# Kernel optimization log

Measured on AMD Instinct MI355X. Metric: run time of the kernel, lower is better.

The kernel has to match this reference:

```python
import jax, jax.numpy as jnp
import numpy as np

B, H_WIN, W_WIN = 2048, 8, 8
N = H_WIN * W_WIN            # tokens per window = 64
C = 384                      # channels
HEADS, HEAD_DIM = 12, 32
E = HEADS * HEAD_DIM         # embedding channels = 384
EPS = 1e-5


def _relative_position_indices(h, w):
    coords = np.stack(np.meshgrid(np.arange(h), np.arange(w), indexing='ij')).reshape(2, -1)  # [2, N]
    rel = coords[:, :, None] - coords[:, None, :]      # [2, N, N]
    rel = rel.transpose(1, 2, 0).astype(np.int64)      # [N, N, 2]
    rel[..., 0] = (rel[..., 0] + h - 1) * (2 * w - 1)
    rel[..., 1] += w - 1
    return rel.sum(-1)                                 # [N, N] in [0, (2h-1)(2w-1))


def setup_inputs() -> dict:
    key = jax.random.key(0)
    ks = jax.random.split(key, 6)
    x = jax.random.normal(ks[0], (B, N, C), dtype=jnp.float32)
    ln_g = jnp.ones((C,), jnp.float32)
    ln_b = jnp.zeros((C,), jnp.float32)
    w_qkv = jax.random.normal(ks[1], (3 * E, C), jnp.float32) * (1.0 / np.sqrt(C))
    w_out = jax.random.normal(ks[2], (C, E), jnp.float32) * (1.0 / np.sqrt(E))
    b_out = jnp.zeros((C,), jnp.float32)
    n_bias = (2 * H_WIN - 1) * (2 * W_WIN - 1)
    bias_table = jax.random.truncated_normal(ks[3], -2.0, 2.0, (n_bias, HEADS), jnp.float32) * 0.02
    rel_idx = jnp.asarray(_relative_position_indices(H_WIN, W_WIN))  # [N, N] int64
    return {"x": x, "ln_g": ln_g, "ln_b": ln_b, "w_qkv": w_qkv,
            "w_out": w_out, "b_out": b_out, "bias_table": bias_table, "rel_idx": rel_idx}


def reference(x, ln_g, ln_b, w_qkv, w_out, b_out, bias_table, rel_idx):
    # pre-norm
    mu = jnp.mean(x, axis=-1, keepdims=True)
    var = jnp.var(x, axis=-1, keepdims=True)
    xn = (x - mu) * jax.lax.rsqrt(var + EPS) * ln_g + ln_b
    # qkv projection (no bias)
    qkv = jnp.einsum('bnc,ec->bne', xn, w_qkv)                     # [B, N, 3E]
    qkv = qkv.reshape(x.shape[0], N, 3, HEADS, HEAD_DIM)
    q, k, v = (qkv[:, :, i].transpose(0, 2, 1, 3) for i in range(3))  # each [B, h, N, d]
    scale = 1.0 / np.sqrt(HEAD_DIM)
    scores = jnp.einsum('bhnd,bhmd->bhnm', q * scale, k)           # [B, h, N, N]
    # gather learned relative-position bias per (n, m) pair
    bias = bias_table[rel_idx]                                     # [N, N, h]
    scores = scores + bias.transpose(2, 0, 1)[None]                # broadcast over B
    p = jax.nn.softmax(scores, axis=-1)
    out = jnp.einsum('bhnm,bhmd->bhnd', p, v)                      # [B, h, N, d]
    out = out.transpose(0, 2, 1, 3).reshape(x.shape[0], N, E)
    return jnp.einsum('bne,ce->bnc', out, w_out) + b_out
```

## Files before the change

kernel.cpp:

```cpp
#include <hip/hip_runtime.h>
#include <hip/hip_bf16.h>


#define NTOK  64
#define CCH   384
#define NH    12
#define HD    32
#define EPSV  1e-5f
#define SCALEQ 0.17677669529663687f

#define WQP_ELEMS (72 * 12 * 64 * 8)
#define WOP_ELEMS (24 * 12 * 64 * 8)
#define BLUTP_ELEMS (12 * 4 * 4 * 64 * 4)

typedef __attribute__((ext_vector_type(8))) short  short8;
typedef __attribute__((ext_vector_type(4))) short  short4v;
typedef __attribute__((ext_vector_type(4))) float  float4v;
typedef __attribute__((ext_vector_type(4))) int    int4v;

__device__ __forceinline__ unsigned short f2bf(float f) {
    union { float f; unsigned int i; } v; v.f = f;
    unsigned int r = v.i + 0x7fffu + ((v.i >> 16) & 1u);
    return (unsigned short)(r >> 16);
}
__device__ __forceinline__ unsigned int pack2bf(float lo, float hi) {
    return (unsigned int)f2bf(lo) | ((unsigned int)f2bf(hi) << 16);
}

__global__ void prep_kernel(const float* __restrict__ w_qkv_f,
                            const float* __restrict__ w_out_f,
                            const float* __restrict__ bias_tab,
                            const int*   __restrict__ rel_idx,
                            unsigned short* __restrict__ wqp,
                            unsigned short* __restrict__ wop,
                            float* __restrict__ blutp) {
    const int stride = gridDim.x * blockDim.x;
    const int tid = blockIdx.x * blockDim.x + threadIdx.x;
    for (int i = tid; i < WQP_ELEMS; i += stride) {
        const int t = i / 6144, rem = i % 6144;
        const int kk = rem >> 9, rem2 = rem & 511;
        const int lane = rem2 >> 3, e = rem2 & 7;
        wqp[i] = f2bf(w_qkv_f[(16 * t + (lane & 15)) * CCH + 32 * kk + 8 * (lane >> 4) + e]);
    }
    for (int i = tid; i < WOP_ELEMS; i += stride) {
        const int t = i / 6144, rem = i % 6144;
        const int kk = rem >> 9, rem2 = rem & 511;
        const int lane = rem2 >> 3, e = rem2 & 7;
        wop[i] = f2bf(w_out_f[(16 * t + (lane & 15)) * CCH + 32 * kk + 8 * (lane >> 4) + e]);
    }
    for (int i = tid; i < BLUTP_ELEMS; i += stride) {
        const int r = i & 3, lane = (i >> 2) & 63;
        const int kt = (i >> 8) & 3, tt = (i >> 10) & 3, h = i >> 12;
        const int token = 16 * tt + (lane & 15);
        const int key   = 16 * kt + 4 * (lane >> 4) + r;
        blutp[i] = bias_tab[rel_idx[token * 64 + key] * NH + h];
    }
}

__global__ __launch_bounds__(512, 2)
void fused_win_mha(const float* __restrict__ x,
                   const float* __restrict__ ln_g,
                   const float* __restrict__ ln_b,
                   const float* __restrict__ b_out,
                   const unsigned short* __restrict__ wqp,
                   const unsigned short* __restrict__ wop,
                   const float* __restrict__ blutp,
                   float* __restrict__ out)
{
    const int b    = blockIdx.x;
    const int t    = threadIdx.x;
    const int wav  = t >> 6;
    const int lane = t & 63;
    const int l4   = lane >> 4;
    const int lc   = lane & 15;
    const int lh   = wav >> 1;
    const int mh   = wav & 1;

    __shared__ unsigned short xnp[4 * 12 * 64 * 8];
    __shared__ unsigned short qp [4 * 4 * 64 * 8];
    __shared__ unsigned short kp [4 * 4 * 64 * 8];
    __shared__ unsigned short vp [4 * 2 * 2 * 64 * 8];
    __shared__ unsigned short attp[4 * 4 * 64 * 8];

    {
        const int row = t >> 3, seg = t & 7;
        const float* xr = x + (b * NTOK + row) * CCH + seg * 48;
        float vals[48];
        float s = 0.f, s2 = 0.f;
        #pragma unroll
        for (int i = 0; i < 12; ++i) {
            float4v v = *(const float4v*)(xr + i * 4);
            #pragma unroll
            for (int j = 0; j < 4; ++j) {
                float f = v[j];
                vals[i * 4 + j] = f; s += f; s2 += f * f;
            }
        }
        s += __shfl_xor(s, 1); s2 += __shfl_xor(s2, 1);
        s += __shfl_xor(s, 2); s2 += __shfl_xor(s2, 2);
        s += __shfl_xor(s, 4); s2 += __shfl_xor(s2, 4);
        const float mu   = s * (1.f / CCH);
        const float rstd = rsqrtf(s2 * (1.f / CCH) - mu * mu + EPSV);
        #pragma unroll
        for (int u = 0; u < 6; ++u) {
            const int col0 = seg * 48 + u * 8;
            short8 w;
            #pragma unroll
            for (int e2 = 0; e2 < 2; ++e2) {
                float4v gv = *(const float4v*)(ln_g + col0 + e2 * 4);
                float4v bv = *(const float4v*)(ln_b + col0 + e2 * 4);
                #pragma unroll
                for (int j = 0; j < 4; ++j)
                    w[e2 * 4 + j] = (short)f2bf((vals[u * 8 + e2 * 4 + j] - mu) * rstd * gv[j] + bv[j]);
            }
            const int idx = ((((row >> 4) * 12 + (col0 >> 5)) << 9)
                             + ((((col0 >> 3) & 3) * 16 + (row & 15)) << 3));
            *(short8*)&xnp[idx] = w;
        }
    }
    __syncthreads();

    float4v facc[4][3];
    #pragma unroll
    for (int mt = 0; mt < 4; ++mt)
        #pragma unroll
        for (int j = 0; j < 3; ++j)
            facc[mt][j] = (float4v){0.f, 0.f, 0.f, 0.f};

    auto do_gemm2 = [&](int g) {
        #pragma unroll
        for (int ks = 0; ks < 4; ++ks) {
            short8 aG[4];
            #pragma unroll
            for (int mt = 0; mt < 4; ++mt)
                aG[mt] = *(const short8*)&attp[((mt * 4 + ks) << 9) + (lane << 3)];
            #pragma unroll
            for (int j2 = 0; j2 < 3; ++j2) {
                const int tile = 3 * wav + j2;
                short8 bG = *(const short8*)&wop[((tile * 12 + 4 * g + ks) << 9) + (lane << 3)];
                #pragma unroll
                for (int mt = 0; mt < 4; ++mt)
                    facc[mt][j2] = __builtin_amdgcn_mfma_f32_16x16x32_bf16(aG[mt], bG, facc[mt][j2], 0, 0, 0);
            }
        }
    };

    for (int grp = 0; grp < 3; ++grp) {
        const int h = 4 * grp + lh;

        if (grp > 0) do_gemm2(grp - 1);

        float4v acc[3][4];
        #pragma unroll
        for (int n = 0; n < 3; ++n)
            #pragma unroll
            for (int m = 0; m < 4; ++m)
                acc[n][m] = (float4v){0.f, 0.f, 0.f, 0.f};

        int tile_[3], mat_[3], half_[3];
        #pragma unroll
        for (int ntl = 0; ntl < 3; ++ntl) {
            const int part = 3 * mh + ntl;
            mat_[ntl] = part >> 1; half_[ntl] = part & 1;
            tile_[ntl] = mat_[ntl] * 24 + h * 2 + half_[ntl];
        }
        for (int kk = 0; kk < 12; ++kk) {
            short8 aF[4];
            #pragma unroll
            for (int mt = 0; mt < 4; ++mt)
                aF[mt] = *(const short8*)&xnp[(((mt * 12 + kk) << 9)) + (lane << 3)];
            #pragma unroll
            for (int ntl = 0; ntl < 3; ++ntl) {
                short8 bF = *(const short8*)&wqp[((tile_[ntl] * 12 + kk) << 9) + (lane << 3)];
                #pragma unroll
                for (int mt = 0; mt < 4; ++mt)
                    acc[ntl][mt] = __builtin_amdgcn_mfma_f32_16x16x32_bf16(aF[mt], bF, acc[ntl][mt], 0, 0, 0);
            }
        }

        float4v bb[2][4];
        #pragma unroll
        for (int j = 0; j < 2; ++j)
            #pragma unroll
            for (int kt = 0; kt < 4; ++kt)
                bb[j][kt] = *(const float4v*)(blutp + ((((h * 4 + (2 * mh + j)) * 4 + kt) << 6) + lane) * 4);

        #pragma unroll
        for (int ntl = 0; ntl < 3; ++ntl) {
            const int mat = mat_[ntl], half = half_[ntl];
            #pragma unroll
            for (int mt = 0; mt < 4; ++mt) {
                if (mat == 0) {
                    const int base = ((lh * 4 + mt) << 9) + ((2 * half + (lc >> 3)) << 7) + (lc & 7);
                    #pragma unroll
                    for (int r = 0; r < 4; ++r)
                        qp[base + ((4 * l4 + r) << 3)] = f2bf(acc[ntl][mt][r] * SCALEQ);
                } else if (mat == 1) {
                    const int base = ((lh * 4 + mt) << 9) + ((2 * half + (lc >> 3)) << 7) + (lc & 7);
                    #pragma unroll
                    for (int r = 0; r < 4; ++r)
                        kp[base + ((4 * l4 + r) << 3)] = f2bf(acc[ntl][mt][r]);
                } else {
                    short4v pk4;
                    #pragma unroll
                    for (int r = 0; r < 4; ++r)
                        pk4[r] = (short)f2bf(acc[ntl][mt][r]);
                    const int addr = (((lh * 2 + half) * 2 + (mt >> 1)) << 9)
                                   + ((((mt & 1) * 2 + (l4 >> 1)) * 16 + lc) << 3)
                                   + ((l4 & 1) << 2);
                    *(short4v*)&vp[addr] = pk4;
                }
            }
        }
        __syncthreads();

        float sv[2][4][4];
        #pragma unroll
        for (int j = 0; j < 2; ++j) {
            short8 qf = *(const short8*)&qp[((lh * 4 + (2 * mh + j)) << 9) + (lane << 3)];
            #pragma unroll
            for (int kt = 0; kt < 4; ++kt) {
                short8 kf = *(const short8*)&kp[((lh * 4 + kt) << 9) + (lane << 3)];
                float4v sres = __builtin_amdgcn_mfma_f32_16x16x32_bf16(
                    kf, qf, (float4v){0.f, 0.f, 0.f, 0.f}, 0, 0, 0);
                #pragma unroll
                for (int r = 0; r < 4; ++r) sv[j][kt][r] = sres[r];
            }
        }
        unsigned int pk2[2][4][2];
        #pragma unroll
        for (int j = 0; j < 2; ++j) {
            float m = -1e30f;
            #pragma unroll
            for (int kt = 0; kt < 4; ++kt) {
                #pragma unroll
                for (int r = 0; r < 4; ++r) {
                    sv[j][kt][r] += bb[j][kt][r];
                    m = fmaxf(m, sv[j][kt][r]);
                }
            }
            m = fmaxf(m, __shfl_xor(m, 16));
            m = fmaxf(m, __shfl_xor(m, 32));
            float s = 0.f;
            #pragma unroll
            for (int kt = 0; kt < 4; ++kt)
                #pragma unroll
                for (int r = 0; r < 4; ++r) {
                    float pe = __expf(sv[j][kt][r] - m);
                    sv[j][kt][r] = pe; s += pe;
                }
            s += __shfl_xor(s, 16);
            s += __shfl_xor(s, 32);
            const float rinv = 1.f / s;
            #pragma unroll
            for (int kt = 0; kt < 4; ++kt) {
                pk2[j][kt][0] = pack2bf(sv[j][kt][0] * rinv, sv[j][kt][1] * rinv);
                pk2[j][kt][1] = pack2bf(sv[j][kt][2] * rinv, sv[j][kt][3] * rinv);
            }
        }
        short8 af[2][2];
        {
            const int src0 = lc + 16 * (2 * (l4 & 1));
            const int src1 = src0 + 16;
            const bool hi  = ((l4 >> 1) & 1) != 0;
            #pragma unroll
            for (int j = 0; j < 2; ++j) {
                #pragma unroll
                for (int kk2 = 0; kk2 < 2; ++kk2) {
                    const int ka = 2 * kk2, kb = 2 * kk2 + 1;
                    unsigned int a0a = (unsigned int)__shfl((int)pk2[j][ka][0], src0);
                    unsigned int a0b = (unsigned int)__shfl((int)pk2[j][kb][0], src0);
                    unsigned int a1a = (unsigned int)__shfl((int)pk2[j][ka][1], src0);
                    unsigned int a1b = (unsigned int)__shfl((int)pk2[j][kb][1], src0);
                    unsigned int a2a = (unsigned int)__shfl((int)pk2[j][ka][0], src1);
                    unsigned int a2b = (unsigned int)__shfl((int)pk2[j][kb][0], src1);
                    unsigned int a3a = (unsigned int)__shfl((int)pk2[j][ka][1], src1);
                    unsigned int a3b = (unsigned int)__shfl((int)pk2[j][kb][1], src1);
                    int4v iv;
                    iv[0] = (int)(hi ? a0b : a0a);
                    iv[1] = (int)(hi ? a1b : a1a);
                    iv[2] = (int)(hi ? a2b : a2a);
                    iv[3] = (int)(hi ? a3b : a3a);
                    af[j][kk2] = __builtin_bit_cast(short8, iv);
                }
            }
        }

        float4v o[2][2];
        #pragma unroll
        for (int j = 0; j < 2; ++j)
            #pragma unroll
            for (int nt = 0; nt < 2; ++nt)
                o[j][nt] = (float4v){0.f, 0.f, 0.f, 0.f};
        #pragma unroll
        for (int kk2 = 0; kk2 < 2; ++kk2) {
            #pragma unroll
            for (int nt = 0; nt < 2; ++nt) {
                short8 vf = *(const short8*)&vp[(((lh * 2 + nt) * 2 + kk2) << 9) + (lane << 3)];
                #pragma unroll
                for (int j = 0; j < 2; ++j)
                    o[j][nt] = __builtin_amdgcn_mfma_f32_16x16x32_bf16(af[j][kk2], vf, o[j][nt], 0, 0, 0);
            }
        }
        #pragma unroll
        for (int j = 0; j < 2; ++j) {
            #pragma unroll
            for (int nt = 0; nt < 2; ++nt) {
                const int base = (((2 * mh + j) * 4 + lh) << 9) + ((2 * nt + (lc >> 3)) << 7) + (lc & 7);
                #pragma unroll
                for (int r = 0; r < 4; ++r)
                    attp[base + ((4 * l4 + r) << 3)] = f2bf(o[j][nt][r]);
            }
        }
        __syncthreads();
    }
    do_gemm2(2);

    {
        float* ob = out + b * (NTOK * CCH);
        #pragma unroll
        for (int mt = 0; mt < 4; ++mt) {
            #pragma unroll
            for (int j2 = 0; j2 < 3; ++j2) {
                const int c = 16 * (3 * wav + j2) + lc;
                const float bo = b_out[c];
                #pragma unroll
                for (int r = 0; r < 4; ++r)
                    ob[(16 * mt + 4 * l4 + r) * CCH + c] = facc[mt][j2][r] + bo;
            }
        }
    }
}

extern "C" void kernel_launch(void* const* d_in, const int* in_sizes, int n_in,
                              void* d_out, int out_size, void* d_ws, size_t ws_size,
                              hipStream_t stream) {
    const float* x     = (const float*)d_in[0];
    const float* ln_g  = (const float*)d_in[1];
    const float* ln_b  = (const float*)d_in[2];
    const float* w_qkv = (const float*)d_in[3];
    const float* w_out = (const float*)d_in[4];
    const float* b_out = (const float*)d_in[5];
    const float* btab  = (const float*)d_in[6];
    const int*   ridx  = (const int*)d_in[7];
    float*       out   = (float*)d_out;

    unsigned short* wqp   = (unsigned short*)d_ws;
    unsigned short* wop   = wqp + WQP_ELEMS;
    float*          blutp = (float*)(wop + WOP_ELEMS);

    prep_kernel<<<512, 256, 0, stream>>>(w_qkv, w_out, btab, ridx, wqp, wop, blutp);
    fused_win_mha<<<2048, 512, 0, stream>>>(x, ln_g, ln_b, b_out, wqp, wop, blutp, out);
}
```

Measured before the change: 342.3 us.

## Software-pipeline QKV GEMM with previous group's softmax, PV and output GEMM

Result: faster. 315.2 us (-7.9%).

```diff
diff --git a/kernel.cpp b/kernel.cpp
--- a/kernel.cpp
+++ b/kernel.cpp
@@ -127,139 +127,37 @@
         for (int j = 0; j < 3; ++j)
             facc[mt][j] = (float4v){0.f, 0.f, 0.f, 0.f};
 
-    auto do_gemm2 = [&](int g) {
-        #pragma unroll
-        for (int ks = 0; ks < 4; ++ks) {
-            short8 aG[4];
-            #pragma unroll
-            for (int mt = 0; mt < 4; ++mt)
-                aG[mt] = *(const short8*)&attp[((mt * 4 + ks) << 9) + (lane << 3)];
-            #pragma unroll
-            for (int j2 = 0; j2 < 3; ++j2) {
-                const int tile = 3 * wav + j2;
-                short8 bG = *(const short8*)&wop[((tile * 12 + 4 * g + ks) << 9) + (lane << 3)];
-                #pragma unroll
-                for (int mt = 0; mt < 4; ++mt)
-                    facc[mt][j2] = __builtin_amdgcn_mfma_f32_16x16x32_bf16(aG[mt], bG, facc[mt][j2], 0, 0, 0);
-            }
-        }
-    };
-
-    for (int grp = 0; grp < 3; ++grp) {
-        const int h = 4 * grp + lh;
-
-        if (grp > 0) do_gemm2(grp - 1);
-
-        float4v acc[3][4];
-        #pragma unroll
-        for (int n = 0; n < 3; ++n)
-            #pragma unroll
-            for (int m = 0; m < 4; ++m)
-                acc[n][m] = (float4v){0.f, 0.f, 0.f, 0.f};
-
-        int tile_[3], mat_[3], half_[3];
-        #pragma unroll
-        for (int ntl = 0; ntl < 3; ++ntl) {
-            const int part = 3 * mh + ntl;
-            mat_[ntl] = part >> 1; half_[ntl] = part & 1;
-            tile_[ntl] = mat_[ntl] * 24 + h * 2 + half_[ntl];
-        }
-        for (int kk = 0; kk < 12; ++kk) {
-            short8 aF[4];
-            #pragma unroll
-            for (int mt = 0; mt < 4; ++mt)
-                aF[mt] = *(const short8*)&xnp[(((mt * 12 + kk) << 9)) + (lane << 3)];
-            #pragma unroll
-            for (int ntl = 0; ntl < 3; ++ntl) {
-                short8 bF = *(const short8*)&wqp[((tile_[ntl] * 12 + kk) << 9) + (lane << 3)];
-                #pragma unroll
-                for (int mt = 0; mt < 4; ++mt)
-                    acc[ntl][mt] = __builtin_amdgcn_mfma_f32_16x16x32_bf16(aF[mt], bF, acc[ntl][mt], 0, 0, 0);
-            }
-        }
-
-        float4v bb[2][4];
-        #pragma unroll
-        for (int j = 0; j < 2; ++j)
-            #pragma unroll
-            for (int kt = 0; kt < 4; ++kt)
-                bb[j][kt] = *(const float4v*)(blutp + ((((h * 4 + (2 * mh + j)) * 4 + kt) << 6) + lane) * 4);
-
-        #pragma unroll
-        for (int ntl = 0; ntl < 3; ++ntl) {
-            const int mat = mat_[ntl], half = half_[ntl];
-            #pragma unroll
-            for (int mt = 0; mt < 4; ++mt) {
-                if (mat == 0) {
-                    const int base = ((lh * 4 + mt) << 9) + ((2 * half + (lc >> 3)) << 7) + (lc & 7);
-                    #pragma unroll
-                    for (int r = 0; r < 4; ++r)
-                        qp[base + ((4 * l4 + r) << 3)] = f2bf(acc[ntl][mt][r] * SCALEQ);
-                } else if (mat == 1) {
-                    const int base = ((lh * 4 + mt) << 9) + ((2 * half + (lc >> 3)) << 7) + (lc & 7);
-                    #pragma unroll
-                    for (int r = 0; r < 4; ++r)
-                        kp[base + ((4 * l4 + r) << 3)] = f2bf(acc[ntl][mt][r]);
-                } else {
-                    short4v pk4;
-                    #pragma unroll
-                    for (int r = 0; r < 4; ++r)
-                        pk4[r] = (short)f2bf(acc[ntl][mt][r]);
-                    const int addr = (((lh * 2 + half) * 2 + (mt >> 1)) << 9)
-                                   + ((((mt & 1) * 2 + (l4 >> 1)) * 16 + lc) << 3)
-                                   + ((l4 & 1) << 2);
-                    *(short4v*)&vp[addr] = pk4;
-                }
-            }
-        }
-        __syncthreads();
-
-        float sv[2][4][4];
-        #pragma unroll
-        for (int j = 0; j < 2; ++j) {
-            short8 qf = *(const short8*)&qp[((lh * 4 + (2 * mh + j)) << 9) + (lane << 3)];
-            #pragma unroll
-            for (int kt = 0; kt < 4; ++kt) {
-                short8 kf = *(const short8*)&kp[((lh * 4 + kt) << 9) + (lane << 3)];
-                float4v sres = __builtin_amdgcn_mfma_f32_16x16x32_bf16(
-                    kf, qf, (float4v){0.f, 0.f, 0.f, 0.f}, 0, 0, 0);
-                #pragma unroll
-                for (int r = 0; r < 4; ++r) sv[j][kt][r] = sres[r];
-            }
-        }
-        unsigned int pk2[2][4][2];
-        #pragma unroll
-        for (int j = 0; j < 2; ++j) {
-            float m = -1e30f;
-            #pragma unroll
-            for (int kt = 0; kt < 4; ++kt) {
-                #pragma unroll
-                for (int r = 0; r < 4; ++r) {
-                    sv[j][kt][r] += bb[j][kt][r];
-                    m = fmaxf(m, sv[j][kt][r]);
-                }
-            }
-            m = fmaxf(m, __shfl_xor(m, 16));
-            m = fmaxf(m, __shfl_xor(m, 32));
-            float s = 0.f;
-            #pragma unroll
-            for (int kt = 0; kt < 4; ++kt)
-                #pragma unroll
-                for (int r = 0; r < 4; ++r) {
-                    float pe = __expf(sv[j][kt][r] - m);
-                    sv[j][kt][r] = pe; s += pe;
-                }
-            s += __shfl_xor(s, 16);
-            s += __shfl_xor(s, 32);
-            const float rinv = 1.f / s;
-            #pragma unroll
-            for (int kt = 0; kt < 4; ++kt) {
-                pk2[j][kt][0] = pack2bf(sv[j][kt][0] * rinv, sv[j][kt][1] * rinv);
-                pk2[j][kt][1] = pack2bf(sv[j][kt][2] * rinv, sv[j][kt][3] * rinv);
-            }
-        }
+    float sv[2][4][4];
+    float mx[2];
+
+    #pragma unroll
+    for (int it = 0; it < 4; ++it) {
         short8 af[2][2];
-        {
+        if (it > 0) {
+            unsigned int pk2[2][4][2];
+            #pragma unroll
+            for (int j = 0; j < 2; ++j) {
+                float sk[4];
+                #pragma unroll
+                for (int kt = 0; kt < 4; ++kt) {
+                    float pe0 = __expf(sv[j][kt][0] - mx[j]);
+                    float pe1 = __expf(sv[j][kt][1] - mx[j]);
+                    float pe2 = __expf(sv[j][kt][2] - mx[j]);
+                    float pe3 = __expf(sv[j][kt][3] - mx[j]);
+                    sv[j][kt][0] = pe0; sv[j][kt][1] = pe1;
+                    sv[j][kt][2] = pe2; sv[j][kt][3] = pe3;
+                    sk[kt] = (pe0 + pe1) + (pe2 + pe3);
+                }
+                float s = (sk[0] + sk[1]) + (sk[2] + sk[3]);
+                s += __shfl_xor(s, 16);
+                s += __shfl_xor(s, 32);
+                const float rinv = 1.f / s;
+                #pragma unroll
+                for (int kt = 0; kt < 4; ++kt) {
+                    pk2[j][kt][0] = pack2bf(sv[j][kt][0] * rinv, sv[j][kt][1] * rinv);
+                    pk2[j][kt][1] = pack2bf(sv[j][kt][2] * rinv, sv[j][kt][3] * rinv);
+                }
+            }
             const int src0 = lc + 16 * (2 * (l4 & 1));
             const int src1 = src0 + 16;
             const bool hi  = ((l4 >> 1) & 1) != 0;
@@ -286,35 +184,147 @@
             }
         }
 
-        float4v o[2][2];
-        #pragma unroll
-        for (int j = 0; j < 2; ++j)
-            #pragma unroll
-            for (int nt = 0; nt < 2; ++nt)
-                o[j][nt] = (float4v){0.f, 0.f, 0.f, 0.f};
-        #pragma unroll
-        for (int kk2 = 0; kk2 < 2; ++kk2) {
-            #pragma unroll
-            for (int nt = 0; nt < 2; ++nt) {
-                short8 vf = *(const short8*)&vp[(((lh * 2 + nt) * 2 + kk2) << 9) + (lane << 3)];
-                #pragma unroll
-                for (int j = 0; j < 2; ++j)
-                    o[j][nt] = __builtin_amdgcn_mfma_f32_16x16x32_bf16(af[j][kk2], vf, o[j][nt], 0, 0, 0);
-            }
-        }
-        #pragma unroll
-        for (int j = 0; j < 2; ++j) {
-            #pragma unroll
-            for (int nt = 0; nt < 2; ++nt) {
-                const int base = (((2 * mh + j) * 4 + lh) << 9) + ((2 * nt + (lc >> 3)) << 7) + (lc & 7);
-                #pragma unroll
-                for (int r = 0; r < 4; ++r)
-                    attp[base + ((4 * l4 + r) << 3)] = f2bf(o[j][nt][r]);
+        float4v acc[3][4];
+        int tile_[3], mat_[3], half_[3];
+        if (it < 3) {
+            const int h = 4 * it + lh;
+            #pragma unroll
+            for (int n = 0; n < 3; ++n)
+                #pragma unroll
+                for (int m = 0; m < 4; ++m)
+                    acc[n][m] = (float4v){0.f, 0.f, 0.f, 0.f};
+            #pragma unroll
+            for (int ntl = 0; ntl < 3; ++ntl) {
+                const int part = 3 * mh + ntl;
+                mat_[ntl] = part >> 1; half_[ntl] = part & 1;
+                tile_[ntl] = mat_[ntl] * 24 + h * 2 + half_[ntl];
+            }
+            #pragma unroll
+            for (int kk = 0; kk < 12; ++kk) {
+                short8 aF[4];
+                #pragma unroll
+                for (int mt = 0; mt < 4; ++mt)
+                    aF[mt] = *(const short8*)&xnp[((mt * 12 + kk) << 9) + (lane << 3)];
+                #pragma unroll
+                for (int ntl = 0; ntl < 3; ++ntl) {
+                    short8 bF = *(const short8*)&wqp[((tile_[ntl] * 12 + kk) << 9) + (lane << 3)];
+                    #pragma unroll
+                    for (int mt = 0; mt < 4; ++mt)
+                        acc[ntl][mt] = __builtin_amdgcn_mfma_f32_16x16x32_bf16(aF[mt], bF, acc[ntl][mt], 0, 0, 0);
+                }
+            }
+        }
+
+        if (it > 0) {
+            float4v o[2][2];
+            #pragma unroll
+            for (int j = 0; j < 2; ++j)
+                #pragma unroll
+                for (int nt = 0; nt < 2; ++nt)
+                    o[j][nt] = (float4v){0.f, 0.f, 0.f, 0.f};
+            #pragma unroll
+            for (int kk2 = 0; kk2 < 2; ++kk2) {
+                #pragma unroll
+                for (int nt = 0; nt < 2; ++nt) {
+                    short8 vf = *(const short8*)&vp[(((lh * 2 + nt) * 2 + kk2) << 9) + (lane << 3)];
+                    #pragma unroll
+                    for (int j = 0; j < 2; ++j)
+                        o[j][nt] = __builtin_amdgcn_mfma_f32_16x16x32_bf16(af[j][kk2], vf, o[j][nt], 0, 0, 0);
+                }
+            }
+            #pragma unroll
+            for (int j = 0; j < 2; ++j) {
+                #pragma unroll
+                for (int nt = 0; nt < 2; ++nt) {
+                    const int base = (((2 * mh + j) * 4 + lh) << 9) + ((2 * nt + (lc >> 3)) << 7) + (lc & 7);
+                    #pragma unroll
+                    for (int r = 0; r < 4; ++r)
+                        attp[base + ((4 * l4 + r) << 3)] = f2bf(o[j][nt][r]);
+                }
             }
         }
         __syncthreads();
-    }
-    do_gemm2(2);
+
+        if (it > 0) {
+            const int g = it - 1;
+            #pragma unroll
+            for (int ks = 0; ks < 4; ++ks) {
+                short8 aG[4];
+                #pragma unroll
+                for (int mt = 0; mt < 4; ++mt)
+                    aG[mt] = *(const short8*)&attp[((mt * 4 + ks) << 9) + (lane << 3)];
+                #pragma unroll
+                for (int j2 = 0; j2 < 3; ++j2) {
+                    short8 bG = *(const short8*)&wop[(((3 * wav + j2) * 12 + 4 * g + ks) << 9) + (lane << 3)];
+                    #pragma unroll
+                    for (int mt = 0; mt < 4; ++mt)
+                        facc[mt][j2] = __builtin_amdgcn_mfma_f32_16x16x32_bf16(aG[mt], bG, facc[mt][j2], 0, 0, 0);
+                }
+            }
+        }
+        if (it < 3) {
+            #pragma unroll
+            for (int ntl = 0; ntl < 3; ++ntl) {
+                const int mat = mat_[ntl], half = half_[ntl];
+                #pragma unroll
+                for (int mt = 0; mt < 4; ++mt) {
+                    if (mat == 0) {
+                        const int base = ((lh * 4 + mt) << 9) + ((2 * half + (lc >> 3)) << 7) + (lc & 7);
+                        #pragma unroll
+                        for (int r = 0; r < 4; ++r)
+                            qp[base + ((4 * l4 + r) << 3)] = f2bf(acc[ntl][mt][r] * SCALEQ);
+                    } else if (mat == 1) {
+                        const int base = ((lh * 4 + mt) << 9) + ((2 * half + (lc >> 3)) << 7) + (lc & 7);
+                        #pragma unroll
+                        for (int r = 0; r < 4; ++r)
+                            kp[base + ((4 * l4 + r) << 3)] = f2bf(acc[ntl][mt][r]);
+                    } else {
+                        short4v pk4;
+                        #pragma unroll
+                        for (int r = 0; r < 4; ++r)
+                            pk4[r] = (short)f2bf(acc[ntl][mt][r]);
+                        const int addr = (((lh * 2 + half) * 2 + (mt >> 1)) << 9)
+                                       + ((((mt & 1) * 2 + (l4 >> 1)) * 16 + lc) << 3)
+                                       + ((l4 & 1) << 2);
+                        *(short4v*)&vp[addr] = pk4;
+                    }
+                }
+            }
+        }
+        __syncthreads();
+
+        if (it < 3) {
+            const int h = 4 * it + lh;
+            #pragma unroll
+            for (int j = 0; j < 2; ++j) {
+                short8 qf = *(const short8*)&qp[((lh * 4 + (2 * mh + j)) << 9) + (lane << 3)];
+                #pragma unroll
+                for (int kt = 0; kt < 4; ++kt) {
+                    short8 kf = *(const short8*)&kp[((lh * 4 + kt) << 9) + (lane << 3)];
+                    float4v sres = __builtin_amdgcn_mfma_f32_16x16x32_bf16(
+                        kf, qf, (float4v){0.f, 0.f, 0.f, 0.f}, 0, 0, 0);
+                    #pragma unroll
+                    for (int r = 0; r < 4; ++r) sv[j][kt][r] = sres[r];
+                }
+            }
+            #pragma unroll
+            for (int j = 0; j < 2; ++j) {
+                float m = -1e30f;
+                #pragma unroll
+                for (int kt = 0; kt < 4; ++kt) {
+                    const float4v bb = *(const float4v*)(blutp + ((((h * 4 + (2 * mh + j)) * 4 + kt) << 6) + lane) * 4);
+                    #pragma unroll
+                    for (int r = 0; r < 4; ++r) {
+                        sv[j][kt][r] += bb[r];
+                        m = fmaxf(m, sv[j][kt][r]);
+                    }
+                }
+                m = fmaxf(m, __shfl_xor(m, 16));
+                m = fmaxf(m, __shfl_xor(m, 32));
+                mx[j] = m;
+            }
+        }
+    }
 
     {
         float* ob = out + b * (NTOK * CCH);
```
